# Optimization experiments

Measured on AMD Instinct MI355X. Metric: run time of the kernel, lower is better.

The kernel has to match this reference:

```python
import jax, jax.numpy as jnp
import numpy as np

B, S, I, R, O = 32, 4096, 64, 1024, 8
SPECTRAL_RADIUS = 0.95


def setup_inputs() -> dict:
    key = jax.random.key(0)
    k1, k2, k3, k4 = jax.random.split(key, 4)
    x = jax.random.normal(k1, (B, S, I), dtype=jnp.float32)
    W_in = jax.random.uniform(k2, (R, I), dtype=jnp.float32) - 0.5
    W_res = jax.random.uniform(k3, (R, R), dtype=jnp.float32) - 0.5
    # rescale W_res so its spectral radius equals SPECTRAL_RADIUS (as in __init__)
    radius = SPECTRAL_RADIUS / float(np.max(np.abs(np.linalg.eigvals(np.asarray(W_res)))))
    W_res = W_res * jnp.float32(radius)
    # original inits W_out to zeros; use small random values so output is non-trivial
    W_out = jax.random.normal(k4, (O, R + I), dtype=jnp.float32) * 0.02
    return {"x": x, "W_in": W_in, "W_res": W_res, "W_out": W_out}


def reference(x, W_in, W_res, W_out):
    # Precompute input drive for all timesteps: [B, S, R]
    pre = jnp.einsum('bsi,ri->bsr', x, W_in)

    def step(r, p_t):
        # r: [B, R], p_t: [B, R]
        r = jnp.tanh(p_t + r @ W_res.T)
        return r, r

    r0 = jnp.zeros((x.shape[0], W_res.shape[0]), dtype=x.dtype)
    _, rs = jax.lax.scan(step, r0, jnp.swapaxes(pre, 0, 1))  # rs: [S, B, R]
    rs = jnp.swapaxes(rs, 0, 1)                               # [B, S, R]
    feats = jnp.concatenate([x, rs], axis=-1)                 # [B, S, I+R]
    out = jnp.einsum('bsf,of->bso', feats, W_out)             # [B, S, O]
    return jnp.squeeze(out)
```

## Files before the change

kernel.cpp:

```cpp
#include <hip/hip_runtime.h>
#include <hip/hip_fp16.h>
#include <math.h>


#define NS 4096
#define NI 64
#define NR 1024
#define NO 8
#define NB 32
#define NGRP 8
#define GPP 32
#define CPG 4
#define WROWS 32
#define NT 512
#define XPAD 68

typedef __fp16 h2 __attribute__((ext_vector_type(2)));
union UH2 { unsigned u; h2 h; };

#define ATSU(p,v) __hip_atomic_store((p), (v), __ATOMIC_RELAXED, __HIP_MEMORY_SCOPE_AGENT)
#define ATLU(p)   __hip_atomic_load((p), __ATOMIC_RELAXED, __HIP_MEMORY_SCOPE_AGENT)
#define ATAU(p,v) __hip_atomic_fetch_add((p), (v), __ATOMIC_RELAXED, __HIP_MEMORY_SCOPE_AGENT)

static __device__ __forceinline__ h2 u2h(unsigned u) { UH2 t; t.u = u; return t.h; }

static __device__ __forceinline__ float fast_tanh(float x) {
  x = fminf(fmaxf(x, -20.f), 20.f);
  float e = __builtin_amdgcn_exp2f(x * 2.8853900817779268f);
  return (e - 1.0f) * __builtin_amdgcn_rcpf(e + 1.0f);
}

__global__ void init_cnt_kernel(unsigned int* cnt) {
  cnt[threadIdx.x] = 0u;
  cnt[threadIdx.x + 1024] = 0u;
}

__global__ __launch_bounds__(NT)
__attribute__((amdgpu_waves_per_eu(2, 2)))
void esn_scan(const float* __restrict__ x, const float* __restrict__ Win,
              const float* __restrict__ Wres, const float* __restrict__ Wout,
              float* __restrict__ out, unsigned int* __restrict__ cnt,
              unsigned int* __restrict__ rbuf_h)
{
  extern __shared__ float dynpad[];
  const int wg  = blockIdx.x;
  const int g   = wg & 7;
  const int m   = wg >> 3;
  const int tid = threadIdx.x;
  const int w   = tid >> 6;
  const int l   = tid & 63;

  __shared__ unsigned r_h[CPG][NR / 2];
  __shared__ float x_lds[3][CPG][XPAD];
  __shared__ float win_s[WROWS][XPAD];
  __shared__ unsigned woutr_h[NO][NR / 2];
  __shared__ float woutx_s[NO][NI];

  if (x[0] == 1234.5678f) { dynpad[tid] = 1.f; out[tid] = dynpad[tid ^ 1]; }

  h2 wh[32];
  {
    const int grow0 = 32 * m + 4 * w;
    #pragma unroll
    for (int r = 0; r < 4; ++r)
      #pragma unroll
      for (int s = 0; s < 4; ++s) {
        float4 t4 = *(const float4*)&Wres[(size_t)(grow0 + r) * NR + 4 * l + 256 * s];
        wh[(r * 4 + s) * 2 + 0] = __builtin_amdgcn_cvt_pkrtz(t4.x, t4.y);
        wh[(r * 4 + s) * 2 + 1] = __builtin_amdgcn_cvt_pkrtz(t4.z, t4.w);
      }
  }
  for (int idx = tid; idx < WROWS * NI; idx += NT) {
    int rr = idx >> 6, ii = idx & 63;
    win_s[rr][ii] = Win[(32 * m + rr) * NI + ii];
  }
  for (int idx = tid; idx < NO * (NR / 2); idx += NT) {
    int o = idx >> 9, p = idx & 511;
    UH2 t; t.h = __builtin_amdgcn_cvt_pkrtz(Wout[o * (NI + NR) + NI + 2 * p],
                                            Wout[o * (NI + NR) + NI + 2 * p + 1]);
    woutr_h[o][p] = t.u;
  }
  if (tid < NO * NI) {
    int o = tid >> 6, ii = tid & 63;
    woutx_s[o][ii] = Wout[o * (NI + NR) + ii];
  }
  if (tid < 256) {
    const int c = tid >> 6, ii = tid & 63;
    x_lds[0][c][ii] = x[(size_t)(4 * g + c) * NS * NI + ii];
  }
  __syncthreads();

  unsigned int* bcp = cnt + (g * 4 + (m & 3)) * 64;
  unsigned int* pol = cnt + g * 4 * 64;

  for (int t = 0; t < NS; ++t) {
    const int par = t & 1, pprev = par ^ 1;

    unsigned uv0, uv1, uv2, uv3;
    if (t > 0) {
      const unsigned* rq = rbuf_h + (size_t)pprev * NB * (NR / 2)
                                  + (size_t)(4 * g) * (NR / 2);
      uv0 = ATLU(rq + tid);
      uv1 = ATLU(rq + 512 + tid);
      uv2 = ATLU(rq + 1024 + tid);
      uv3 = ATLU(rq + 1536 + tid);
    } else {
      uv0 = uv1 = uv2 = uv3 = 0u;
    }

    float pin;
    {
      const int p = l & 15;
      const int prow = 4 * w + (p >> 2);
      const int pc = p & 3;
      const int cb = (l >> 4) * 16;
      const float* wr = &win_s[prow][cb];
      const float* xr = &x_lds[t % 3][pc][cb];
      float4 a0 = *(const float4*)&wr[0];
      float4 a1 = *(const float4*)&wr[4];
      float4 a2 = *(const float4*)&wr[8];
      float4 a3 = *(const float4*)&wr[12];
      float4 b0 = *(const float4*)&xr[0];
      float4 b1 = *(const float4*)&xr[4];
      float4 b2 = *(const float4*)&xr[8];
      float4 b3 = *(const float4*)&xr[12];
      pin = a0.x * b0.x;
      pin = fmaf(a0.y, b0.y, pin); pin = fmaf(a0.z, b0.z, pin);
      pin = fmaf(a0.w, b0.w, pin);
      pin = fmaf(a1.x, b1.x, pin); pin = fmaf(a1.y, b1.y, pin);
      pin = fmaf(a1.z, b1.z, pin); pin = fmaf(a1.w, b1.w, pin);
      pin = fmaf(a2.x, b2.x, pin); pin = fmaf(a2.y, b2.y, pin);
      pin = fmaf(a2.z, b2.z, pin); pin = fmaf(a2.w, b2.w, pin);
      pin = fmaf(a3.x, b3.x, pin); pin = fmaf(a3.y, b3.y, pin);
      pin = fmaf(a3.z, b3.z, pin); pin = fmaf(a3.w, b3.w, pin);
      pin += __shfl_xor(pin, 16);
      pin += __shfl_xor(pin, 32);
    }

    r_h[0][tid] = uv0; r_h[1][tid] = uv1;
    r_h[2][tid] = uv2; r_h[3][tid] = uv3;
    __syncthreads();

    float acc[4][4];
    #pragma unroll
    for (int r = 0; r < 4; ++r)
      #pragma unroll
      for (int c = 0; c < 4; ++c) acc[r][c] = 0.f;
    #pragma unroll
    for (int s = 0; s < 4; ++s) {
      uint2 q0 = *(const uint2*)&r_h[0][2 * l + 128 * s];
      uint2 q1 = *(const uint2*)&r_h[1][2 * l + 128 * s];
      uint2 q2 = *(const uint2*)&r_h[2][2 * l + 128 * s];
      uint2 q3 = *(const uint2*)&r_h[3][2 * l + 128 * s];
      #pragma unroll
      for (int r = 0; r < 4; ++r) {
        const h2 wa = wh[(r * 4 + s) * 2 + 0];
        const h2 wb = wh[(r * 4 + s) * 2 + 1];
        acc[r][0] = __builtin_amdgcn_fdot2(wa, u2h(q0.x), acc[r][0], false);
        acc[r][0] = __builtin_amdgcn_fdot2(wb, u2h(q0.y), acc[r][0], false);
        acc[r][1] = __builtin_amdgcn_fdot2(wa, u2h(q1.x), acc[r][1], false);
        acc[r][1] = __builtin_amdgcn_fdot2(wb, u2h(q1.y), acc[r][1], false);
        acc[r][2] = __builtin_amdgcn_fdot2(wa, u2h(q2.x), acc[r][2], false);
        acc[r][2] = __builtin_amdgcn_fdot2(wb, u2h(q2.y), acc[r][2], false);
        acc[r][3] = __builtin_amdgcn_fdot2(wa, u2h(q3.x), acc[r][3], false);
        acc[r][3] = __builtin_amdgcn_fdot2(wb, u2h(q3.y), acc[r][3], false);
      }
    }

    float v[16];
    #pragma unroll
    for (int k = 0; k < 16; ++k) v[k] = acc[k >> 2][k & 3];
    #pragma unroll
    for (int lev = 0; lev < 4; ++lev) {
      const int d = 1 << lev;
      const int n = 16 >> lev;
      #pragma unroll
      for (int i = 0; i < n / 2; ++i) {
        float a  = v[2 * i]     + __shfl_xor(v[2 * i],     d);
        float bb = v[2 * i + 1] + __shfl_xor(v[2 * i + 1], d);
        v[i] = (l & d) ? bb : a;
      }
    }
    float dsum = v[0];
    dsum += __shfl_xor(dsum, 16);
    dsum += __shfl_xor(dsum, 32);

    {
      float rv = fast_tanh(dsum + pin);
      float rvo = __shfl_xor(rv, 4);
      if (l < 16 && ((l >> 2) & 1) == 0) {
        const int r = l >> 2, c = l & 3;
        UH2 hp; hp.h = __builtin_amdgcn_cvt_pkrtz(rv, rvo);
        const int pair = 16 * m + 2 * w + (r >> 1);
        ATSU(rbuf_h + (size_t)par * NB * (NR / 2)
                    + (size_t)(4 * g + c) * (NR / 2) + pair, hp.u);
      }
    }

    __syncthreads();
    if (tid == 0) ATAU(bcp, 1u);

    if (t + 1 < NS && tid < 256) {
      const int c = tid >> 6, ii = tid & 63;
      x_lds[(t + 1) % 3][c][ii] = x[((size_t)(4 * g + c) * NS + (t + 1)) * NI + ii];
    }
    if (t > 0 && m == ((t - 1) & 31)) {
      const int grp = tid >> 4;
      const int j   = tid & 15;
      const int c   = grp >> 3, o = grp & 7;
      float s = 0.f;
      #pragma unroll
      for (int k = 0; k < 16; ++k) {
        uint2 rr = *(const uint2*)&r_h[c][32 * k + 2 * j];
        uint2 ww = *(const uint2*)&woutr_h[o][32 * k + 2 * j];
        s = __builtin_amdgcn_fdot2(u2h(rr.x), u2h(ww.x), s, false);
        s = __builtin_amdgcn_fdot2(u2h(rr.y), u2h(ww.y), s, false);
      }
      #pragma unroll
      for (int e = 0; e < 4; ++e)
        s = fmaf(woutx_s[o][4 * j + e], x_lds[(t + 2) % 3][c][4 * j + e], s);
      s += __shfl_xor(s, 1); s += __shfl_xor(s, 2);
      s += __shfl_xor(s, 4); s += __shfl_xor(s, 8);
      if (j == 0) out[((size_t)(4 * g + c) * NS + (t - 1)) * NO + o] = s;
    }

    if (tid == 0) {
      const unsigned tg = 8u * (unsigned)(t + 1);
      for (;;) {
        unsigned u0 = ATLU(pol);
        unsigned u1 = ATLU(pol + 64);
        unsigned u2 = ATLU(pol + 128);
        unsigned u3 = ATLU(pol + 192);
        if (u0 >= tg && u1 >= tg && u2 >= tg && u3 >= tg) break;
      }
    }
    __syncthreads();
  }

  if (m == 31) {
    const int fpar = (NS - 1) & 1;
    const unsigned* rq = rbuf_h + (size_t)fpar * NB * (NR / 2)
                                + (size_t)(4 * g) * (NR / 2);
    r_h[0][tid] = ATLU(rq + tid);
    r_h[1][tid] = ATLU(rq + 512 + tid);
    r_h[2][tid] = ATLU(rq + 1024 + tid);
    r_h[3][tid] = ATLU(rq + 1536 + tid);
    __syncthreads();
    const int grp = tid >> 4;
    const int j   = tid & 15;
    const int c   = grp >> 3, o = grp & 7;
    float s = 0.f;
    #pragma unroll
    for (int k = 0; k < 16; ++k) {
      uint2 rr = *(const uint2*)&r_h[c][32 * k + 2 * j];
      uint2 ww = *(const uint2*)&woutr_h[o][32 * k + 2 * j];
      s = __builtin_amdgcn_fdot2(u2h(rr.x), u2h(ww.x), s, false);
      s = __builtin_amdgcn_fdot2(u2h(rr.y), u2h(ww.y), s, false);
    }
    #pragma unroll
    for (int e = 0; e < 4; ++e)
      s = fmaf(woutx_s[o][4 * j + e], x_lds[(NS - 1) % 3][c][4 * j + e], s);
    s += __shfl_xor(s, 1); s += __shfl_xor(s, 2);
    s += __shfl_xor(s, 4); s += __shfl_xor(s, 8);
    if (j == 0) out[((size_t)(4 * g + c) * NS + (NS - 1)) * NO + o] = s;
  }
}

extern "C" void kernel_launch(void* const* d_in, const int* in_sizes, int n_in,
                              void* d_out, int out_size, void* d_ws, size_t ws_size,
                              hipStream_t stream) {
  const float* x    = (const float*)d_in[0];
  const float* Win  = (const float*)d_in[1];
  const float* Wres = (const float*)d_in[2];
  const float* Wout = (const float*)d_in[3];
  float* out = (float*)d_out;

  char* ws = (char*)d_ws;
  unsigned int* cnt = (unsigned int*)ws;
  unsigned int* rbuf_h = (unsigned int*)(ws + 8192);

  hipLaunchKernelGGL(init_cnt_kernel, dim3(1), dim3(1024), 0, stream, cnt);
  hipLaunchKernelGGL(esn_scan, dim3(256), dim3(NT), 64 * 1024, stream,
                     x, Win, Wres, Wout, out, cnt, rbuf_h);
}
```

Measured before the change: 9.572 ms.

## Replace atomic-add barrier counters with per-block flags and widen state stores

```diff
diff --git a/kernel.cpp b/kernel.cpp
--- a/kernel.cpp
+++ b/kernel.cpp
@@ -18,9 +18,9 @@
 typedef __fp16 h2 __attribute__((ext_vector_type(2)));
 union UH2 { unsigned u; h2 h; };
 
-#define ATSU(p,v) __hip_atomic_store((p), (v), __ATOMIC_RELAXED, __HIP_MEMORY_SCOPE_AGENT)
-#define ATLU(p)   __hip_atomic_load((p), __ATOMIC_RELAXED, __HIP_MEMORY_SCOPE_AGENT)
-#define ATAU(p,v) __hip_atomic_fetch_add((p), (v), __ATOMIC_RELAXED, __HIP_MEMORY_SCOPE_AGENT)
+#define ATSU(p,v)   __hip_atomic_store((p), (v), __ATOMIC_RELAXED, __HIP_MEMORY_SCOPE_AGENT)
+#define ATSU64(p,v) __hip_atomic_store((p), (v), __ATOMIC_RELAXED, __HIP_MEMORY_SCOPE_AGENT)
+#define ATLU(p)     __hip_atomic_load((p), __ATOMIC_RELAXED, __HIP_MEMORY_SCOPE_AGENT)
 
 static __device__ __forceinline__ h2 u2h(unsigned u) { UH2 t; t.u = u; return t.h; }
 
@@ -90,8 +90,7 @@
   }
   __syncthreads();
 
-  unsigned int* bcp = cnt + (g * 4 + (m & 3)) * 64;
-  unsigned int* pol = cnt + g * 4 * 64;
+  unsigned int* flg = cnt + g * 64;
 
   for (int t = 0; t < NS; ++t) {
     const int par = t & 1, pprev = par ^ 1;
@@ -188,21 +187,24 @@
     {
       float rv = fast_tanh(dsum + pin);
       float rvo = __shfl_xor(rv, 4);
-      if (l < 16 && ((l >> 2) & 1) == 0) {
-        const int r = l >> 2, c = l & 3;
-        UH2 hp; hp.h = __builtin_amdgcn_cvt_pkrtz(rv, rvo);
-        const int pair = 16 * m + 2 * w + (r >> 1);
-        ATSU(rbuf_h + (size_t)par * NB * (NR / 2)
-                    + (size_t)(4 * g + c) * (NR / 2) + pair, hp.u);
-      }
-    }
-
-    __syncthreads();
-    if (tid == 0) ATAU(bcp, 1u);
-
-    if (t + 1 < NS && tid < 256) {
-      const int c = tid >> 6, ii = tid & 63;
-      x_lds[(t + 1) % 3][c][ii] = x[((size_t)(4 * g + c) * NS + (t + 1)) * NI + ii];
+      UH2 hp; hp.h = __builtin_amdgcn_cvt_pkrtz(rv, rvo);
+      unsigned hp2 = __shfl_xor(hp.u, 8);
+      if (l < 4) {
+        const int c = l;
+        const size_t idx = (size_t)par * NB * (NR / 2)
+                         + (size_t)(4 * g + c) * (NR / 2) + 16 * m + 2 * w;
+        unsigned long long dbl = ((unsigned long long)hp2 << 32) | (unsigned long long)hp.u;
+        ATSU64((unsigned long long*)(rbuf_h + idx), dbl);
+      }
+    }
+
+    __syncthreads();
+    if (tid == 0) ATSU(flg + m, (unsigned)(t + 1));
+
+    if (t + 1 < NS && tid < 64) {
+      const int c = tid >> 4, q = tid & 15;
+      float4 xv = *(const float4*)&x[((size_t)(4 * g + c) * NS + (t + 1)) * NI + 4 * q];
+      *(float4*)&x_lds[(t + 1) % 3][c][4 * q] = xv;
     }
     if (t > 0 && m == ((t - 1) & 31)) {
       const int grp = tid >> 4;
@@ -225,13 +227,12 @@
     }
 
     if (tid == 0) {
-      const unsigned tg = 8u * (unsigned)(t + 1);
+      const unsigned tg = (unsigned)(t + 1);
       for (;;) {
-        unsigned u0 = ATLU(pol);
-        unsigned u1 = ATLU(pol + 64);
-        unsigned u2 = ATLU(pol + 128);
-        unsigned u3 = ATLU(pol + 192);
-        if (u0 >= tg && u1 >= tg && u2 >= tg && u3 >= tg) break;
+        unsigned ok = 1u;
+        #pragma unroll
+        for (int k = 0; k < 32; ++k) ok &= (ATLU(flg + k) >= tg) ? 1u : 0u;
+        if (ok) break;
       }
     }
     __syncthreads();
```

Measured after the change: 12.09 ms. 26.4% more time.
